# Optimization experiments

Measured on AMD Instinct MI355X. Metric: run time of the kernel, lower is better.

Reference implementation:

```python
import jax, jax.numpy as jnp
import numpy as np

N_EMBD = 1024
N_HEAD = 16


def setup_inputs() -> dict:
    key = jax.random.key(0)
    k1, k2, k3 = jax.random.split(key, 3)
    B, T, C = 4, 2048, N_EMBD
    x = jax.random.normal(k1, (B, T, C), dtype=jnp.float32)
    # params (bias=False)
    w_attn = jax.random.normal(k2, (C, 3 * C), dtype=jnp.float32) * (C ** -0.5)
    w_proj = jax.random.normal(k3, (C, C), dtype=jnp.float32) * (C ** -0.5)
    return {"x": x, "w_attn": w_attn, "w_proj": w_proj}


def reference(x, w_attn, w_proj):
    B, T, C = x.shape
    H = N_HEAD
    hs = C // H
    qkv = x @ w_attn  # [B,T,3C]
    q, k, v = jnp.split(qkv, 3, axis=-1)
    # [B,H,T,hs]
    q = q.reshape(B, T, H, hs).transpose(0, 2, 1, 3)
    k = k.reshape(B, T, H, hs).transpose(0, 2, 1, 3)
    v = v.reshape(B, T, H, hs).transpose(0, 2, 1, 3)
    wei = jnp.einsum('bhqd,bhkd->bhqk', q, k) * (hs ** -0.5)
    causal = jnp.tril(jnp.ones((T, T), dtype=bool))
    wei = jnp.where(causal[None, None], wei, -jnp.inf)
    wei = jax.nn.softmax(wei, axis=-1)
    # dropout p=0.0 -> identity
    y = jnp.einsum('bhqk,bhkd->bhqd', wei, v)
    y = y.transpose(0, 2, 1, 3).reshape(B, T, C)
    return y @ w_proj
```

## Files before the change

kernel.cpp:

```cpp
#include <hip/hip_runtime.h>
#include <math.h>
#include <stdint.h>

#define B_BATCH 4
#define T_SEQ   2048
#define C_EMB   1024
#define NH      16
#define HS      64

typedef _Float16 half_t;
typedef __attribute__((ext_vector_type(8))) _Float16 half8;
typedef __attribute__((ext_vector_type(4))) _Float16 half4;
typedef __attribute__((ext_vector_type(2))) __fp16 pk16x2;
typedef __attribute__((ext_vector_type(4))) float f32x4;

static __device__ __forceinline__ f32x4 mfma_k16(half4 a, half4 b, f32x4 c) {
#if __has_builtin(__builtin_amdgcn_mfma_f32_16x16x16f16)
    return __builtin_amdgcn_mfma_f32_16x16x16f16(a, b, c, 0, 0, 0);
#else
    half8 a8 = {a.x, a.y, a.z, a.w, (_Float16)0, (_Float16)0, (_Float16)0, (_Float16)0};
    half8 b8 = {b.x, b.y, b.z, b.w, (_Float16)0, (_Float16)0, (_Float16)0, (_Float16)0};
    return __builtin_amdgcn_mfma_f32_16x16x32_f16(a8, b8, c, 0, 0, 0);
#endif
}

static __device__ __forceinline__ void stage16(const void* g, void* lds_base) {
#if __has_builtin(__builtin_amdgcn_global_load_lds)
    __builtin_amdgcn_global_load_lds(
        (const __attribute__((address_space(1))) void*)g,
        (__attribute__((address_space(3))) void*)lds_base, 16, 0, 0);
#else
    const int lane = threadIdx.x & 63;
    ((uint4*)lds_base)[lane] = *(const uint4*)g;
#endif
}

__global__ __launch_bounds__(256) void prep_kernel(const float* __restrict__ x,
                                                   half_t* __restrict__ xh,
                                                   const float* __restrict__ wa,
                                                   half_t* __restrict__ waT,
                                                   const float* __restrict__ wp,
                                                   half_t* __restrict__ wpT) {
    const int blk = blockIdx.x;
    const int tid = threadIdx.x;

    if (blk < 4096) {
        const int i = blk * 256 + tid;
        const float4 a = *(const float4*)(x + (size_t)i * 8);
        const float4 b = *(const float4*)(x + (size_t)i * 8 + 4);
        const pk16x2 h0 = __builtin_amdgcn_cvt_pkrtz(a.x, a.y);
        const pk16x2 h1 = __builtin_amdgcn_cvt_pkrtz(a.z, a.w);
        const pk16x2 h2 = __builtin_amdgcn_cvt_pkrtz(b.x, b.y);
        const pk16x2 h3 = __builtin_amdgcn_cvt_pkrtz(b.z, b.w);
        half8 o = {(_Float16)h0.x, (_Float16)h0.y, (_Float16)h1.x, (_Float16)h1.y,
                   (_Float16)h2.x, (_Float16)h2.y, (_Float16)h3.x, (_Float16)h3.y};
        *(half8*)(xh + (size_t)i * 8) = o;
        return;
    }

    const float* W;
    half_t* WT;
    int K, N, bb;
    if (blk < 4096 + 768) {
        bb = blk - 4096; W = wa; WT = waT; K = 1024; N = 3072;
    } else {
        bb = blk - 4864; W = wp; WT = wpT; K = 1024; N = 1024;
    }
    const int ntiles = N / 64;
    const int n0 = (bb % ntiles) * 64;
    const int k0 = (bb / ntiles) * 64;

    __shared__ float t[64][65];
    const int r = tid >> 4, c4 = (tid & 15) * 4;
#pragma unroll
    for (int p = 0; p < 4; ++p) {
        const float4 g = *(const float4*)(W + (size_t)(k0 + p * 16 + r) * N + n0 + c4);
        t[p * 16 + r][c4 + 0] = g.x;
        t[p * 16 + r][c4 + 1] = g.y;
        t[p * 16 + r][c4 + 2] = g.z;
        t[p * 16 + r][c4 + 3] = g.w;
    }
    __syncthreads();
#pragma unroll
    for (int p = 0; p < 4; ++p) {
        const int n = p * 16 + r;
        half4 s = {(_Float16)t[c4 + 0][n], (_Float16)t[c4 + 1][n],
                   (_Float16)t[c4 + 2][n], (_Float16)t[c4 + 3][n]};
        *(half4*)(WT + (size_t)(n0 + n) * K + k0 + c4) = s;
    }
}

#define BK2 64

__global__ __launch_bounds__(512, 2) void gemm256(const half_t* __restrict__ A,
                                                  const half_t* __restrict__ Bt,
                                                  half_t* __restrict__ Cout,
                                                  int M, int N, int K) {
    __shared__ __align__(16) half_t SM[65536];

    const int tid  = threadIdx.x;
    const int lane = tid & 63;
    const int wid  = tid >> 6;
    const int l16  = lane & 15;
    const int quad = lane >> 4;

    const int nwg = gridDim.x;
    const int cpx = nwg >> 3;
    const int bid = (blockIdx.x & 7) * cpx + (blockIdx.x >> 3);
    const int nbx = N >> 8;
    const int bx = bid % nbx;
    const int by = bid / nbx;
    const size_t m0 = (size_t)by << 8;
    const size_t n0 = (size_t)bx << 8;

    const int warpM = (wid >> 2) * 128;
    const int wn    = (wid & 3) * 64;
    const int NTk   = K >> 6;

    const int srow = tid >> 3;
    const int scsw = (tid & 7) ^ (srow & 7);
    const half_t* gAs = A  + (m0 + srow) * (size_t)K + scsw * 8;
    const half_t* gBs = Bt + (n0 + srow) * (size_t)K + scsw * 8;

    f32x4 acc[8][4];
#pragma unroll
    for (int i = 0; i < 8; ++i)
#pragma unroll
        for (int j = 0; j < 4; ++j) acc[i][j] = (f32x4){0.f, 0.f, 0.f, 0.f};

    auto ldA = [&](const half_t* Ab, int mt, int kk) -> half8 {
        const int r = warpM + mt * 16 + l16;
        const int c = (kk * 4 + quad) ^ (l16 & 7);
        return *(const half8*)(Ab + r * 64 + c * 8);
    };
    auto ldB = [&](const half_t* Bb, int nt, int kk) -> half8 {
        const int r = wn + nt * 16 + l16;
        const int c = (kk * 4 + quad) ^ (l16 & 7);
        return *(const half8*)(Bb + r * 64 + c * 8);
    };

#pragma unroll
    for (int s = 0; s < 4; ++s)
        stage16(gAs + (size_t)(s * 64) * K, SM + s * 4096 + wid * 512);
#pragma unroll
    for (int s = 0; s < 4; ++s)
        stage16(gBs + (size_t)(s * 64) * K, SM + 16384 + s * 4096 + wid * 512);
    if (NTk > 1) {
#pragma unroll
        for (int s = 0; s < 4; ++s)
            stage16(gBs + (size_t)(s * 64) * K + BK2, SM + 49152 + s * 4096 + wid * 512);
        asm volatile("s_waitcnt vmcnt(4)" ::: "memory");
    } else {
        asm volatile("s_waitcnt vmcnt(0)" ::: "memory");
    }
    __builtin_amdgcn_s_barrier();
    __builtin_amdgcn_sched_barrier(0);

    auto tile_body = [&](int t, half_t* Ac, half_t* Bc, half_t* An) {
        const int kA = (t + 1) * BK2;
        const int kB = (t + 2) * BK2;
        const bool doA = (t + 1) < NTk;
        const bool doB = (t + 2) < NTk;

        half8 fb[4][2];

        if (doA) {
            stage16(gAs + (size_t)(0 * 64) * K + kA, An + 0 * 4096 + wid * 512);
            stage16(gAs + (size_t)(1 * 64) * K + kA, An + 1 * 4096 + wid * 512);
        }
#pragma unroll
        for (int nt = 0; nt < 4; ++nt) {
            fb[nt][0] = ldB(Bc, nt, 0);
            fb[nt][1] = ldB(Bc, nt, 1);
        }
        {
            half8 a00 = ldA(Ac, 0, 0), a01 = ldA(Ac, 0, 1);
            half8 a10 = ldA(Ac, 1, 0), a11 = ldA(Ac, 1, 1);
            __builtin_amdgcn_s_barrier();
            __builtin_amdgcn_s_setprio(1);
#pragma unroll
            for (int nt = 0; nt < 4; ++nt) {
                acc[0][nt] = __builtin_amdgcn_mfma_f32_16x16x32_f16(a00, fb[nt][0], acc[0][nt], 0, 0, 0);
                acc[0][nt] = __builtin_amdgcn_mfma_f32_16x16x32_f16(a01, fb[nt][1], acc[0][nt], 0, 0, 0);
                acc[1][nt] = __builtin_amdgcn_mfma_f32_16x16x32_f16(a10, fb[nt][0], acc[1][nt], 0, 0, 0);
                acc[1][nt] = __builtin_amdgcn_mfma_f32_16x16x32_f16(a11, fb[nt][1], acc[1][nt], 0, 0, 0);
            }
            __builtin_amdgcn_s_setprio(0);
        }
        if (doA) {
            stage16(gAs + (size_t)(2 * 64) * K + kA, An + 2 * 4096 + wid * 512);
            stage16(gAs + (size_t)(3 * 64) * K + kA, An + 3 * 4096 + wid * 512);
        }
        {
            half8 a00 = ldA(Ac, 2, 0), a01 = ldA(Ac, 2, 1);
            half8 a10 = ldA(Ac, 3, 0), a11 = ldA(Ac, 3, 1);
            __builtin_amdgcn_s_barrier();
            __builtin_amdgcn_s_setprio(1);
#pragma unroll
            for (int nt = 0; nt < 4; ++nt) {
                acc[2][nt] = __builtin_amdgcn_mfma_f32_16x16x32_f16(a00, fb[nt][0], acc[2][nt], 0, 0, 0);
                acc[2][nt] = __builtin_amdgcn_mfma_f32_16x16x32_f16(a01, fb[nt][1], acc[2][nt], 0, 0, 0);
                acc[3][nt] = __builtin_amdgcn_mfma_f32_16x16x32_f16(a10, fb[nt][0], acc[3][nt], 0, 0, 0);
                acc[3][nt] = __builtin_amdgcn_mfma_f32_16x16x32_f16(a11, fb[nt][1], acc[3][nt], 0, 0, 0);
            }
            __builtin_amdgcn_s_setprio(0);
        }
        if (doB) {
            stage16(gBs + (size_t)(0 * 64) * K + kB, Bc + 0 * 4096 + wid * 512);
            stage16(gBs + (size_t)(1 * 64) * K + kB, Bc + 1 * 4096 + wid * 512);
        }
        {
            half8 a00 = ldA(Ac, 4, 0), a01 = ldA(Ac, 4, 1);
            half8 a10 = ldA(Ac, 5, 0), a11 = ldA(Ac, 5, 1);
            __builtin_amdgcn_s_barrier();
            __builtin_amdgcn_s_setprio(1);
#pragma unroll
            for (int nt = 0; nt < 4; ++nt) {
                acc[4][nt] = __builtin_amdgcn_mfma_f32_16x16x32_f16(a00, fb[nt][0], acc[4][nt], 0, 0, 0);
                acc[4][nt] = __builtin_amdgcn_mfma_f32_16x16x32_f16(a01, fb[nt][1], acc[4][nt], 0, 0, 0);
                acc[5][nt] = __builtin_amdgcn_mfma_f32_16x16x32_f16(a10, fb[nt][0], acc[5][nt], 0, 0, 0);
                acc[5][nt] = __builtin_amdgcn_mfma_f32_16x16x32_f16(a11, fb[nt][1], acc[5][nt], 0, 0, 0);
            }
            __builtin_amdgcn_s_setprio(0);
        }
        if (doB) {
            stage16(gBs + (size_t)(2 * 64) * K + kB, Bc + 2 * 4096 + wid * 512);
            stage16(gBs + (size_t)(3 * 64) * K + kB, Bc + 3 * 4096 + wid * 512);
        }
        {
            half8 a00 = ldA(Ac, 6, 0), a01 = ldA(Ac, 6, 1);
            half8 a10 = ldA(Ac, 7, 0), a11 = ldA(Ac, 7, 1);
            __builtin_amdgcn_s_barrier();
            __builtin_amdgcn_s_setprio(1);
#pragma unroll
            for (int nt = 0; nt < 4; ++nt) {
                acc[6][nt] = __builtin_amdgcn_mfma_f32_16x16x32_f16(a00, fb[nt][0], acc[6][nt], 0, 0, 0);
                acc[6][nt] = __builtin_amdgcn_mfma_f32_16x16x32_f16(a01, fb[nt][1], acc[6][nt], 0, 0, 0);
                acc[7][nt] = __builtin_amdgcn_mfma_f32_16x16x32_f16(a10, fb[nt][0], acc[7][nt], 0, 0, 0);
                acc[7][nt] = __builtin_amdgcn_mfma_f32_16x16x32_f16(a11, fb[nt][1], acc[7][nt], 0, 0, 0);
            }
            __builtin_amdgcn_s_setprio(0);
        }
        if (doB) {
            asm volatile("s_waitcnt vmcnt(4)" ::: "memory");
        } else if (doA) {
            asm volatile("s_waitcnt vmcnt(0)" ::: "memory");
        }
        __builtin_amdgcn_s_barrier();
        __builtin_amdgcn_sched_barrier(0);
    };

    for (int tt = 0; tt < NTk; tt += 2) {
        tile_body(tt, SM, SM + 16384, SM + 32768);
        if (tt + 1 < NTk)
            tile_body(tt + 1, SM + 32768, SM + 49152, SM);
    }

    __syncthreads();
    float* cw = (float*)SM + wid * 1024;
    const int rrow = lane >> 2;
    const int cseg = (lane & 3) * 16;
#pragma unroll
    for (int mt = 0; mt < 8; ++mt) {
#pragma unroll
        for (int nt = 0; nt < 4; ++nt)
            *(f32x4*)&cw[(nt * 16 + l16) * 16 + quad * 4] = acc[mt][nt];
        half_t tmp[16];
#pragma unroll
        for (int jj = 0; jj < 16; ++jj)
            tmp[jj] = (half_t)cw[(cseg + jj) * 16 + rrow];
        half_t* dst = Cout + (m0 + warpM + mt * 16 + rrow) * (size_t)N + n0 + wn + cseg;
        *(half8*)(dst)     = *(const half8*)(tmp);
        *(half8*)(dst + 8) = *(const half8*)(tmp + 8);
    }
}

__global__ __launch_bounds__(512, 2) void gemm128f(const half_t* __restrict__ A,
                                                   const half_t* __restrict__ Bt,
                                                   float* __restrict__ Cout,
                                                   int M, int N, int K) {
    __shared__ __align__(16) half_t SM[49152];

    const int tid  = threadIdx.x;
    const int lane = tid & 63;
    const int wid  = tid >> 6;
    const int l16  = lane & 15;
    const int quad = lane >> 4;

    const int nwg = gridDim.x;
    const int cpx = nwg >> 3;
    const int bid = (blockIdx.x & 7) * cpx + (blockIdx.x >> 3);
    const int nbx = N >> 8;
    const int bx = bid % nbx;
    const int by = bid / nbx;
    const size_t m0 = (size_t)by << 7;
    const size_t n0 = (size_t)bx << 8;

    const int warpM = (wid >> 2) * 64;
    const int wn    = (wid & 3) * 64;
    const int NTk   = K >> 6;

    const int srow = tid >> 3;
    const int scsw = (tid & 7) ^ (srow & 7);
    const half_t* gAs = A  + (m0 + srow) * (size_t)K + scsw * 8;
    const half_t* gBs = Bt + (n0 + srow) * (size_t)K + scsw * 8;

    half_t* const A0 = SM;
    half_t* const B0 = SM + 8192;
    half_t* const A1 = SM + 24576;
    half_t* const B1 = SM + 32768;

    f32x4 acc[4][4];
#pragma unroll
    for (int i = 0; i < 4; ++i)
#pragma unroll
        for (int j = 0; j < 4; ++j) acc[i][j] = (f32x4){0.f, 0.f, 0.f, 0.f};

    auto ldA = [&](const half_t* Ab, int mt, int kk) -> half8 {
        const int r = warpM + mt * 16 + l16;
        const int c = (kk * 4 + quad) ^ (l16 & 7);
        return *(const half8*)(Ab + r * 64 + c * 8);
    };
    auto ldB = [&](const half_t* Bb, int nt, int kk) -> half8 {
        const int r = wn + nt * 16 + l16;
        const int c = (kk * 4 + quad) ^ (l16 & 7);
        return *(const half8*)(Bb + r * 64 + c * 8);
    };

#pragma unroll
    for (int s = 0; s < 2; ++s)
        stage16(gAs + (size_t)(s * 64) * K, A0 + s * 4096 + wid * 512);
#pragma unroll
    for (int s = 0; s < 4; ++s)
        stage16(gBs + (size_t)(s * 64) * K, B0 + s * 4096 + wid * 512);
    if (NTk > 1) {
#pragma unroll
        for (int s = 0; s < 4; ++s)
            stage16(gBs + (size_t)(s * 64) * K + BK2, B1 + s * 4096 + wid * 512);
        asm volatile("s_waitcnt vmcnt(4)" ::: "memory");
    } else {
        asm volatile("s_waitcnt vmcnt(0)" ::: "memory");
    }
    __builtin_amdgcn_s_barrier();
    __builtin_amdgcn_sched_barrier(0);

    auto tile_body = [&](int t, half_t* Ac, half_t* Bc, half_t* An) {
        const int kA = (t + 1) * BK2;
        const int kB = (t + 2) * BK2;
        const bool doA = (t + 1) < NTk;
        const bool doB = (t + 2) < NTk;

        half8 fb[4][2];

        if (doA) {
            stage16(gAs + (size_t)(0 * 64) * K + kA, An + 0 * 4096 + wid * 512);
            stage16(gAs + (size_t)(1 * 64) * K + kA, An + 1 * 4096 + wid * 512);
        }
#pragma unroll
        for (int nt = 0; nt < 4; ++nt) {
            fb[nt][0] = ldB(Bc, nt, 0);
            fb[nt][1] = ldB(Bc, nt, 1);
        }
        {
            half8 a00 = ldA(Ac, 0, 0), a01 = ldA(Ac, 0, 1);
            half8 a10 = ldA(Ac, 1, 0), a11 = ldA(Ac, 1, 1);
            __builtin_amdgcn_s_barrier();
            __builtin_amdgcn_s_setprio(1);
#pragma unroll
            for (int nt = 0; nt < 4; ++nt) {
                acc[0][nt] = __builtin_amdgcn_mfma_f32_16x16x32_f16(a00, fb[nt][0], acc[0][nt], 0, 0, 0);
                acc[0][nt] = __builtin_amdgcn_mfma_f32_16x16x32_f16(a01, fb[nt][1], acc[0][nt], 0, 0, 0);
                acc[1][nt] = __builtin_amdgcn_mfma_f32_16x16x32_f16(a10, fb[nt][0], acc[1][nt], 0, 0, 0);
                acc[1][nt] = __builtin_amdgcn_mfma_f32_16x16x32_f16(a11, fb[nt][1], acc[1][nt], 0, 0, 0);
            }
            __builtin_amdgcn_s_setprio(0);
        }
        if (doB) {
#pragma unroll
            for (int s = 0; s < 4; ++s)
                stage16(gBs + (size_t)(s * 64) * K + kB, Bc + s * 4096 + wid * 512);
        }
        {
            half8 a00 = ldA(Ac, 2, 0), a01 = ldA(Ac, 2, 1);
            half8 a10 = ldA(Ac, 3, 0), a11 = ldA(Ac, 3, 1);
            __builtin_amdgcn_s_barrier();
            __builtin_amdgcn_s_setprio(1);
#pragma unroll
            for (int nt = 0; nt < 4; ++nt) {
                acc[2][nt] = __builtin_amdgcn_mfma_f32_16x16x32_f16(a00, fb[nt][0], acc[2][nt], 0, 0, 0);
                acc[2][nt] = __builtin_amdgcn_mfma_f32_16x16x32_f16(a01, fb[nt][1], acc[2][nt], 0, 0, 0);
                acc[3][nt] = __builtin_amdgcn_mfma_f32_16x16x32_f16(a10, fb[nt][0], acc[3][nt], 0, 0, 0);
                acc[3][nt] = __builtin_amdgcn_mfma_f32_16x16x32_f16(a11, fb[nt][1], acc[3][nt], 0, 0, 0);
            }
            __builtin_amdgcn_s_setprio(0);
        }
        if (doB) {
            asm volatile("s_waitcnt vmcnt(4)" ::: "memory");
        } else if (doA) {
            asm volatile("s_waitcnt vmcnt(0)" ::: "memory");
        }
        __builtin_amdgcn_s_barrier();
        __builtin_amdgcn_sched_barrier(0);
    };

    for (int tt = 0; tt < NTk; tt += 2) {
        tile_body(tt, A0, B0, A1);
        if (tt + 1 < NTk)
            tile_body(tt + 1, A1, B1, A0);
    }

#pragma unroll
    for (int mt = 0; mt < 4; ++mt)
#pragma unroll
        for (int nt = 0; nt < 4; ++nt)
#pragma unroll
            for (int r = 0; r < 4; ++r) {
                const size_t row = m0 + warpM + mt * 16 + quad * 4 + r;
                const size_t col = n0 + wn + nt * 16 + l16;
                Cout[row * (size_t)N + col] = acc[mt][nt][r];
            }
}

#define SCALE_EXP2 0.18033688f

__global__ __launch_bounds__(256, 2) void attn_mfma(const half_t* __restrict__ qkv,
                                                    half_t* __restrict__ y) {
    __shared__ __align__(16) half_t Kl[64 * 64];
    __shared__ __align__(16) half_t Vt[64 * 64];
    __shared__ float Lstat[128];

    const int tid  = threadIdx.x;
    const int wid  = tid >> 6;
    const int lane = tid & 63;
    const int l16  = lane & 15;
    const int quad = lane >> 4;

    const int L = blockIdx.x;
    const int g = L & 63;
    const int s = L >> 6;
    const int h = g & 15;
    const int b = g >> 4;

    const size_t rs = 3 * C_EMB;
    const half_t* qb = qkv + (size_t)b * T_SEQ * rs + h * HS;
    const half_t* kb = qb + C_EMB;
    const half_t* vb = qb + 2 * C_EMB;

    const int srow = tid >> 2;
    const int scol = (tid & 3) * 16;
    const int sc2  = (tid & 3) * 2;
    const int rp   = tid & 31;
    const int dblk = tid >> 5;

    const int wq = wid * 32;

    auto kswz = [&](int row, int chunk) -> half_t* {
        return Kl + row * 64 + ((chunk ^ (row & 7)) << 3);
    };
    auto vswz = [&](int row, int chunk) -> half_t* {
        return Vt + row * 64 + ((chunk ^ (row & 7)) << 3);
    };

#pragma unroll 1
    for (int j = 0; j < 2; ++j) {
        const int jj = (j == 0) ? (15 - s) : s;
        const int q0 = jj * 128;
        const int ntk = 2 * jj + 2;

        half8 aQ[2][2];
#pragma unroll
        for (int qs = 0; qs < 2; ++qs)
#pragma unroll
            for (int s2 = 0; s2 < 2; ++s2)
                aQ[qs][s2] = *(const half8*)(qb +
                    (size_t)(q0 + wq + qs * 16 + l16) * rs + s2 * 32 + quad * 8);

        const half_t* kptr = kb + (size_t)srow * rs + scol;
        const half_t* vptr = vb + (size_t)(2 * rp) * rs + dblk * 8;
        half8 kp0, kp1;
        uint4 vpa, vpc;
        kp0 = *(const half8*)(kptr);
        kp1 = *(const half8*)(kptr + 8);
        vpa = *(const uint4*)(vptr);
        vpc = *(const uint4*)(vptr + rs);

        f32x4 O[2][4];
#pragma unroll
        for (int qs = 0; qs < 2; ++qs)
#pragma unroll
            for (int dt = 0; dt < 4; ++dt) O[qs][dt] = (f32x4){0.f, 0.f, 0.f, 0.f};
        float lw[2] = {0.f, 0.f};

        for (int kt = 0; kt < ntk; ++kt) {
            __syncthreads();

            *(half8*)kswz(srow, sc2)     = kp0;
            *(half8*)kswz(srow, sc2 + 1) = kp1;
            {
                const uint32_t a0[4] = {vpa.x, vpa.y, vpa.z, vpa.w};
                const uint32_t c0[4] = {vpc.x, vpc.y, vpc.z, vpc.w};
#pragma unroll
                for (int u = 0; u < 4; ++u) {
                    const int d0 = dblk * 8 + 2 * u;
                    const uint32_t w0 = (a0[u] & 0xffffu) | (c0[u] << 16);
                    const uint32_t w1 = (a0[u] >> 16) | (c0[u] & 0xffff0000u);
                    *(uint32_t*)((unsigned short*)vswz(d0,     rp >> 2) + (rp & 3) * 2) = w0;
                    *(uint32_t*)((unsigned short*)vswz(d0 + 1, rp >> 2) + (rp & 3) * 2) = w1;
                }
            }
            __syncthreads();

            if (kt + 1 < ntk) {
                kptr += 64 * rs;
                vptr += 64 * rs;
                kp0 = *(const half8*)(kptr);
                kp1 = *(const half8*)(kptr + 8);
                vpa = *(const uint4*)(vptr);
                vpc = *(const uint4*)(vptr + rs);
            }

            const bool dmask = (kt >= ntk - 2);

#pragma unroll
            for (int mt = 0; mt < 4; ++mt) {
                const half8 aK0 = *(const half8*)kswz(mt * 16 + l16, quad);
                const half8 aK1 = *(const half8*)kswz(mt * 16 + l16, 4 + quad);
                half4 bV[4];
#pragma unroll
                for (int dt = 0; dt < 4; ++dt)
                    bV[dt] = *(const half4*)(vswz(dt * 16 + l16, 2 * mt + (quad >> 1)) +
                                             (quad & 1) * 4);
                const int kbase = kt * 64 + mt * 16 + quad * 4;
#pragma unroll
                for (int qs = 0; qs < 2; ++qs) {
                    f32x4 sa = (f32x4){0.f, 0.f, 0.f, 0.f};
                    sa = __builtin_amdgcn_mfma_f32_16x16x32_f16(aK0, aQ[qs][0], sa, 0, 0, 0);
                    sa = __builtin_amdgcn_mfma_f32_16x16x32_f16(aK1, aQ[qs][1], sa, 0, 0, 0);

                    float p[4];
#pragma unroll
                    for (int r = 0; r < 4; ++r)
                        p[r] = __builtin_amdgcn_exp2f(sa[r] * SCALE_EXP2);
                    if (dmask) {
                        const int qg = q0 + wq + qs * 16 + l16;
#pragma unroll
                        for (int r = 0; r < 4; ++r)
                            if (kbase + r > qg) p[r] = 0.f;
                    }
                    lw[qs] += (p[0] + p[1]) + (p[2] + p[3]);

                    const half4 pa = {(_Float16)p[0], (_Float16)p[1],
                                      (_Float16)p[2], (_Float16)p[3]};
#pragma unroll
                    for (int dt = 0; dt < 4; ++dt)
                        O[qs][dt] = mfma_k16(pa, bV[dt], O[qs][dt]);
                }
            }
        }

#pragma unroll
        for (int qs = 0; qs < 2; ++qs) {
            lw[qs] += __shfl_xor(lw[qs], 16);
            lw[qs] += __shfl_xor(lw[qs], 32);
            if (quad == 0) Lstat[wq + qs * 16 + l16] = lw[qs];
        }
        __syncthreads();

        if (wid < 2) {
#pragma unroll
            for (int qs = 0; qs < 2; ++qs)
#pragma unroll
                for (int r = 0; r < 4; ++r) {
                    const int rowl = wq + qs * 16 + quad * 4 + r;
                    const float inv = 1.f / Lstat[rowl];
#pragma unroll
                    for (int dt = 0; dt < 4; ++dt)
                        *(vswz(rowl, 2 * dt + (l16 >> 3)) + (l16 & 7)) =
                            (half_t)(O[qs][dt][r] * inv);
                }
        }
        __syncthreads();
        {
            half_t* dst = y + ((size_t)b * T_SEQ + q0 + srow) * C_EMB + h * HS + scol;
            *(half8*)(dst)     = *(const half8*)vswz(srow, sc2);
            *(half8*)(dst + 8) = *(const half8*)vswz(srow, sc2 + 1);
        }
        __syncthreads();

        if (wid >= 2) {
#pragma unroll
            for (int qs = 0; qs < 2; ++qs)
#pragma unroll
                for (int r = 0; r < 4; ++r) {
                    const int rowg = wq + qs * 16 + quad * 4 + r;
                    const float inv = 1.f / Lstat[rowg];
#pragma unroll
                    for (int dt = 0; dt < 4; ++dt)
                        *(vswz(rowg - 64, 2 * dt + (l16 >> 3)) + (l16 & 7)) =
                            (half_t)(O[qs][dt][r] * inv);
                }
        }
        __syncthreads();
        {
            half_t* dst = y + ((size_t)b * T_SEQ + q0 + 64 + srow) * C_EMB + h * HS + scol;
            *(half8*)(dst)     = *(const half8*)vswz(srow, sc2);
            *(half8*)(dst + 8) = *(const half8*)vswz(srow, sc2 + 1);
        }
    }
}

extern "C" void kernel_launch(void* const* d_in, const int* in_sizes, int n_in,
                              void* d_out, int out_size, void* d_ws, size_t ws_size,
                              hipStream_t stream) {
    const float* x      = (const float*)d_in[0];
    const float* w_attn = (const float*)d_in[1];
    const float* w_proj = (const float*)d_in[2];
    float* out = (float*)d_out;

    half_t* xh   = (half_t*)d_ws;
    half_t* waT  = xh   + (size_t)8192 * 1024;
    half_t* wpT  = waT  + (size_t)3072 * 1024;
    half_t* qkvh = wpT  + (size_t)1024 * 1024;
    half_t* yh   = qkvh + (size_t)8192 * 3072;

    prep_kernel<<<5120, 256, 0, stream>>>(x, xh, w_attn, waT, w_proj, wpT);

    gemm256<<<dim3(384), 512, 0, stream>>>(xh, waT, qkvh, 8192, 3072, 1024);

    attn_mfma<<<dim3(512), 256, 0, stream>>>(qkvh, yh);

    gemm128f<<<dim3(256), 512, 0, stream>>>(yh, wpT, out, 8192, 1024, 1024);
}
```

Baseline: 249.1 us.

## Shrink QKV GEMM K-tile to 32 with smaller LDS and simpler schedule

Rewrites the QKV projection GEMM to use a K-step of 32 instead of 64. This halves shared memory to 64KB, raises launch bounds to 4 blocks per CU, changes the LDS swizzle for 32-wide rows, and replaces the four interleaved sub-phases (staggered loads plus barriers) with one load-all-then-MFMA phase per tile. The aim is higher occupancy and fewer barriers. In exchange it doubles the number of K iterations and sync points and loses the fine-grained overlap of global loads with MFMAs. Only 384 blocks are launched, so the extra occupancy may not be usable.

```diff
diff --git a/kernel.cpp b/kernel.cpp
--- a/kernel.cpp
+++ b/kernel.cpp
@@ -90,13 +90,11 @@
     }
 }
 
-#define BK2 64
-
-__global__ __launch_bounds__(512, 2) void gemm256(const half_t* __restrict__ A,
-                                                  const half_t* __restrict__ Bt,
-                                                  half_t* __restrict__ Cout,
-                                                  int M, int N, int K) {
-    __shared__ __align__(16) half_t SM[65536];
+__global__ __launch_bounds__(512, 4) void gemm256k(const half_t* __restrict__ A,
+                                                   const half_t* __restrict__ Bt,
+                                                   half_t* __restrict__ Cout,
+                                                   int M, int N, int K) {
+    __shared__ __align__(16) half_t SM[32768];
 
     const int tid  = threadIdx.x;
     const int lane = tid & 63;
@@ -115,41 +113,43 @@
 
     const int warpM = (wid >> 2) * 128;
     const int wn    = (wid & 3) * 64;
-    const int NTk   = K >> 6;
-
-    const int srow = tid >> 3;
-    const int scsw = (tid & 7) ^ (srow & 7);
+    const int NTk   = K >> 5;
+
+    const int srow = tid >> 2;
+    const int scsw = (tid & 3) ^ ((tid >> 3) & 3);
     const half_t* gAs = A  + (m0 + srow) * (size_t)K + scsw * 8;
     const half_t* gBs = Bt + (n0 + srow) * (size_t)K + scsw * 8;
 
+    half_t* const A0 = SM;
+    half_t* const B0 = SM + 8192;
+    half_t* const A1 = SM + 16384;
+    half_t* const B1 = SM + 24576;
+
     f32x4 acc[8][4];
 #pragma unroll
     for (int i = 0; i < 8; ++i)
 #pragma unroll
         for (int j = 0; j < 4; ++j) acc[i][j] = (f32x4){0.f, 0.f, 0.f, 0.f};
 
-    auto ldA = [&](const half_t* Ab, int mt, int kk) -> half8 {
+    auto ldA = [&](const half_t* Ab, int mt) -> half8 {
         const int r = warpM + mt * 16 + l16;
-        const int c = (kk * 4 + quad) ^ (l16 & 7);
-        return *(const half8*)(Ab + r * 64 + c * 8);
-    };
-    auto ldB = [&](const half_t* Bb, int nt, int kk) -> half8 {
+        const int c = quad ^ ((l16 >> 1) & 3);
+        return *(const half8*)(Ab + r * 32 + c * 8);
+    };
+    auto ldB = [&](const half_t* Bb, int nt) -> half8 {
         const int r = wn + nt * 16 + l16;
-        const int c = (kk * 4 + quad) ^ (l16 & 7);
-        return *(const half8*)(Bb + r * 64 + c * 8);
-    };
-
-#pragma unroll
-    for (int s = 0; s < 4; ++s)
-        stage16(gAs + (size_t)(s * 64) * K, SM + s * 4096 + wid * 512);
-#pragma unroll
-    for (int s = 0; s < 4; ++s)
-        stage16(gBs + (size_t)(s * 64) * K, SM + 16384 + s * 4096 + wid * 512);
+        const int c = quad ^ ((l16 >> 1) & 3);
+        return *(const half8*)(Bb + r * 32 + c * 8);
+    };
+
+    stage16(gAs,                        A0 + wid * 512);
+    stage16(gAs + (size_t)128 * K,      A0 + 4096 + wid * 512);
+    stage16(gBs,                        B0 + wid * 512);
+    stage16(gBs + (size_t)128 * K,      B0 + 4096 + wid * 512);
     if (NTk > 1) {
-#pragma unroll
-        for (int s = 0; s < 4; ++s)
-            stage16(gBs + (size_t)(s * 64) * K + BK2, SM + 49152 + s * 4096 + wid * 512);
-        asm volatile("s_waitcnt vmcnt(4)" ::: "memory");
+        stage16(gBs + 32,                    B1 + wid * 512);
+        stage16(gBs + (size_t)128 * K + 32,  B1 + 4096 + wid * 512);
+        asm volatile("s_waitcnt vmcnt(2)" ::: "memory");
     } else {
         asm volatile("s_waitcnt vmcnt(0)" ::: "memory");
     }
@@ -157,92 +157,36 @@
     __builtin_amdgcn_sched_barrier(0);
 
     auto tile_body = [&](int t, half_t* Ac, half_t* Bc, half_t* An) {
-        const int kA = (t + 1) * BK2;
-        const int kB = (t + 2) * BK2;
+        const int kA = (t + 1) * 32;
+        const int kB = (t + 2) * 32;
         const bool doA = (t + 1) < NTk;
         const bool doB = (t + 2) < NTk;
 
-        half8 fb[4][2];
-
         if (doA) {
-            stage16(gAs + (size_t)(0 * 64) * K + kA, An + 0 * 4096 + wid * 512);
-            stage16(gAs + (size_t)(1 * 64) * K + kA, An + 1 * 4096 + wid * 512);
-        }
-#pragma unroll
-        for (int nt = 0; nt < 4; ++nt) {
-            fb[nt][0] = ldB(Bc, nt, 0);
-            fb[nt][1] = ldB(Bc, nt, 1);
-        }
-        {
-            half8 a00 = ldA(Ac, 0, 0), a01 = ldA(Ac, 0, 1);
-            half8 a10 = ldA(Ac, 1, 0), a11 = ldA(Ac, 1, 1);
-            __builtin_amdgcn_s_barrier();
-            __builtin_amdgcn_s_setprio(1);
-#pragma unroll
-            for (int nt = 0; nt < 4; ++nt) {
-                acc[0][nt] = __builtin_amdgcn_mfma_f32_16x16x32_f16(a00, fb[nt][0], acc[0][nt], 0, 0, 0);
-                acc[0][nt] = __builtin_amdgcn_mfma_f32_16x16x32_f16(a01, fb[nt][1], acc[0][nt], 0, 0, 0);
-                acc[1][nt] = __builtin_amdgcn_mfma_f32_16x16x32_f16(a10, fb[nt][0], acc[1][nt], 0, 0, 0);
-                acc[1][nt] = __builtin_amdgcn_mfma_f32_16x16x32_f16(a11, fb[nt][1], acc[1][nt], 0, 0, 0);
-            }
-            __builtin_amdgcn_s_setprio(0);
-        }
-        if (doA) {
-            stage16(gAs + (size_t)(2 * 64) * K + kA, An + 2 * 4096 + wid * 512);
-            stage16(gAs + (size_t)(3 * 64) * K + kA, An + 3 * 4096 + wid * 512);
-        }
-        {
-            half8 a00 = ldA(Ac, 2, 0), a01 = ldA(Ac, 2, 1);
-            half8 a10 = ldA(Ac, 3, 0), a11 = ldA(Ac, 3, 1);
-            __builtin_amdgcn_s_barrier();
-            __builtin_amdgcn_s_setprio(1);
-#pragma unroll
-            for (int nt = 0; nt < 4; ++nt) {
-                acc[2][nt] = __builtin_amdgcn_mfma_f32_16x16x32_f16(a00, fb[nt][0], acc[2][nt], 0, 0, 0);
-                acc[2][nt] = __builtin_amdgcn_mfma_f32_16x16x32_f16(a01, fb[nt][1], acc[2][nt], 0, 0, 0);
-                acc[3][nt] = __builtin_amdgcn_mfma_f32_16x16x32_f16(a10, fb[nt][0], acc[3][nt], 0, 0, 0);
-                acc[3][nt] = __builtin_amdgcn_mfma_f32_16x16x32_f16(a11, fb[nt][1], acc[3][nt], 0, 0, 0);
-            }
-            __builtin_amdgcn_s_setprio(0);
-        }
+            stage16(gAs + kA,                   An + wid * 512);
+            stage16(gAs + (size_t)128 * K + kA, An + 4096 + wid * 512);
+        }
+        half8 fb[4], fa[8];
+#pragma unroll
+        for (int nt = 0; nt < 4; ++nt) fb[nt] = ldB(Bc, nt);
+#pragma unroll
+        for (int mt = 0; mt < 8; ++mt) fa[mt] = ldA(Ac, mt);
+
+        __builtin_amdgcn_s_setprio(1);
+#pragma unroll
+        for (int mt = 0; mt < 8; ++mt)
+#pragma unroll
+            for (int nt = 0; nt < 4; ++nt)
+                acc[mt][nt] = __builtin_amdgcn_mfma_f32_16x16x32_f16(
+                    fa[mt], fb[nt], acc[mt][nt], 0, 0, 0);
+        __builtin_amdgcn_s_setprio(0);
+
+        __builtin_amdgcn_s_barrier();
+
         if (doB) {
-            stage16(gBs + (size_t)(0 * 64) * K + kB, Bc + 0 * 4096 + wid * 512);
-            stage16(gBs + (size_t)(1 * 64) * K + kB, Bc + 1 * 4096 + wid * 512);
-        }
-        {
-            half8 a00 = ldA(Ac, 4, 0), a01 = ldA(Ac, 4, 1);
-            half8 a10 = ldA(Ac, 5, 0), a11 = ldA(Ac, 5, 1);
-            __builtin_amdgcn_s_barrier();
-            __builtin_amdgcn_s_setprio(1);
-#pragma unroll
-            for (int nt = 0; nt < 4; ++nt) {
-                acc[4][nt] = __builtin_amdgcn_mfma_f32_16x16x32_f16(a00, fb[nt][0], acc[4][nt], 0, 0, 0);
-                acc[4][nt] = __builtin_amdgcn_mfma_f32_16x16x32_f16(a01, fb[nt][1], acc[4][nt], 0, 0, 0);
-                acc[5][nt] = __builtin_amdgcn_mfma_f32_16x16x32_f16(a10, fb[nt][0], acc[5][nt], 0, 0, 0);
-                acc[5][nt] = __builtin_amdgcn_mfma_f32_16x16x32_f16(a11, fb[nt][1], acc[5][nt], 0, 0, 0);
-            }
-            __builtin_amdgcn_s_setprio(0);
-        }
-        if (doB) {
-            stage16(gBs + (size_t)(2 * 64) * K + kB, Bc + 2 * 4096 + wid * 512);
-            stage16(gBs + (size_t)(3 * 64) * K + kB, Bc + 3 * 4096 + wid * 512);
-        }
-        {
-            half8 a00 = ldA(Ac, 6, 0), a01 = ldA(Ac, 6, 1);
-            half8 a10 = ldA(Ac, 7, 0), a11 = ldA(Ac, 7, 1);
-            __builtin_amdgcn_s_barrier();
-            __builtin_amdgcn_s_setprio(1);
-#pragma unroll
-            for (int nt = 0; nt < 4; ++nt) {
-                acc[6][nt] = __builtin_amdgcn_mfma_f32_16x16x32_f16(a00, fb[nt][0], acc[6][nt], 0, 0, 0);
-                acc[6][nt] = __builtin_amdgcn_mfma_f32_16x16x32_f16(a01, fb[nt][1], acc[6][nt], 0, 0, 0);
-                acc[7][nt] = __builtin_amdgcn_mfma_f32_16x16x32_f16(a10, fb[nt][0], acc[7][nt], 0, 0, 0);
-                acc[7][nt] = __builtin_amdgcn_mfma_f32_16x16x32_f16(a11, fb[nt][1], acc[7][nt], 0, 0, 0);
-            }
-            __builtin_amdgcn_s_setprio(0);
-        }
-        if (doB) {
-            asm volatile("s_waitcnt vmcnt(4)" ::: "memory");
+            stage16(gBs + kB,                   Bc + wid * 512);
+            stage16(gBs + (size_t)128 * K + kB, Bc + 4096 + wid * 512);
+            asm volatile("s_waitcnt vmcnt(2)" ::: "memory");
         } else if (doA) {
             asm volatile("s_waitcnt vmcnt(0)" ::: "memory");
         }
@@ -251,9 +195,9 @@
     };
 
     for (int tt = 0; tt < NTk; tt += 2) {
-        tile_body(tt, SM, SM + 16384, SM + 32768);
+        tile_body(tt, A0, B0, A1);
         if (tt + 1 < NTk)
-            tile_body(tt + 1, SM + 32768, SM + 49152, SM);
+            tile_body(tt + 1, A1, B1, A0);
     }
 
     __syncthreads();
@@ -274,6 +218,8 @@
         *(half8*)(dst + 8) = *(const half8*)(tmp + 8);
     }
 }
+
+#define BK2 64
 
 __global__ __launch_bounds__(512, 2) void gemm128f(const half_t* __restrict__ A,
                                                    const half_t* __restrict__ Bt,
@@ -625,7 +571,7 @@
 
     prep_kernel<<<5120, 256, 0, stream>>>(x, xh, w_attn, waT, w_proj, wpT);
 
-    gemm256<<<dim3(384), 512, 0, stream>>>(xh, waT, qkvh, 8192, 3072, 1024);
+    gemm256k<<<dim3(384), 512, 0, stream>>>(xh, waT, qkvh, 8192, 3072, 1024);
 
     attn_mfma<<<dim3(512), 256, 0, stream>>>(qkvh, yh);
 
```

Measured after the change: 721.3 us. +189.6%, slower.

## Double-buffer K/V tiles in LDS for attention kernel, one barrier per step

Applied to the files above, without the earlier changes.

Splits the K and V shared-memory tiles into two buffers so the next tile is written to LDS while the current one is consumed by MFMAs. This cuts the per-iteration barriers from two to one and overlaps LDS stores with compute. In exchange it doubles the K/V LDS footprint, to about 32KB per block, which could reduce occupancy. The register prefetch now runs two tiles ahead.

```diff
diff --git a/kernel.cpp b/kernel.cpp
--- a/kernel.cpp
+++ b/kernel.cpp
@@ -425,8 +425,8 @@
 
 __global__ __launch_bounds__(256, 2) void attn_mfma(const half_t* __restrict__ qkv,
                                                     half_t* __restrict__ y) {
-    __shared__ __align__(16) half_t Kl[64 * 64];
-    __shared__ __align__(16) half_t Vt[64 * 64];
+    __shared__ __align__(16) half_t Kl[2][64 * 64];
+    __shared__ __align__(16) half_t Vt[2][64 * 64];
     __shared__ float Lstat[128];
 
     const int tid  = threadIdx.x;
@@ -454,11 +454,11 @@
 
     const int wq = wid * 32;
 
-    auto kswz = [&](int row, int chunk) -> half_t* {
-        return Kl + row * 64 + ((chunk ^ (row & 7)) << 3);
-    };
-    auto vswz = [&](int row, int chunk) -> half_t* {
-        return Vt + row * 64 + ((chunk ^ (row & 7)) << 3);
+    auto kswz = [&](int bf, int row, int chunk) -> half_t* {
+        return Kl[bf] + row * 64 + ((chunk ^ (row & 7)) << 3);
+    };
+    auto vswz = [&](int bf, int row, int chunk) -> half_t* {
+        return Vt[bf] + row * 64 + ((chunk ^ (row & 7)) << 3);
     };
 
 #pragma unroll 1
@@ -484,6 +484,36 @@
         vpa = *(const uint4*)(vptr);
         vpc = *(const uint4*)(vptr + rs);
 
+        auto writeK = [&](int bf) {
+            *(half8*)kswz(bf, srow, sc2)     = kp0;
+            *(half8*)kswz(bf, srow, sc2 + 1) = kp1;
+        };
+        auto writeV = [&](int bf) {
+            const uint32_t a0[4] = {vpa.x, vpa.y, vpa.z, vpa.w};
+            const uint32_t c0[4] = {vpc.x, vpc.y, vpc.z, vpc.w};
+#pragma unroll
+            for (int u = 0; u < 4; ++u) {
+                const int d0 = dblk * 8 + 2 * u;
+                const uint32_t w0 = (a0[u] & 0xffffu) | (c0[u] << 16);
+                const uint32_t w1 = (a0[u] >> 16) | (c0[u] & 0xffff0000u);
+                *(uint32_t*)((unsigned short*)vswz(bf, d0,     rp >> 2) + (rp & 3) * 2) = w0;
+                *(uint32_t*)((unsigned short*)vswz(bf, d0 + 1, rp >> 2) + (rp & 3) * 2) = w1;
+            }
+        };
+
+        __syncthreads();
+        writeK(0);
+        writeV(0);
+        if (ntk > 1) {
+            kptr += 64 * rs;
+            vptr += 64 * rs;
+            kp0 = *(const half8*)(kptr);
+            kp1 = *(const half8*)(kptr + 8);
+            vpa = *(const uint4*)(vptr);
+            vpc = *(const uint4*)(vptr + rs);
+        }
+        __syncthreads();
+
         f32x4 O[2][4];
 #pragma unroll
         for (int qs = 0; qs < 2; ++qs)
@@ -491,44 +521,31 @@
             for (int dt = 0; dt < 4; ++dt) O[qs][dt] = (f32x4){0.f, 0.f, 0.f, 0.f};
         float lw[2] = {0.f, 0.f};
 
+        int cur = 0;
         for (int kt = 0; kt < ntk; ++kt) {
-            __syncthreads();
-
-            *(half8*)kswz(srow, sc2)     = kp0;
-            *(half8*)kswz(srow, sc2 + 1) = kp1;
-            {
-                const uint32_t a0[4] = {vpa.x, vpa.y, vpa.z, vpa.w};
-                const uint32_t c0[4] = {vpc.x, vpc.y, vpc.z, vpc.w};
-#pragma unroll
-                for (int u = 0; u < 4; ++u) {
-                    const int d0 = dblk * 8 + 2 * u;
-                    const uint32_t w0 = (a0[u] & 0xffffu) | (c0[u] << 16);
-                    const uint32_t w1 = (a0[u] >> 16) | (c0[u] & 0xffff0000u);
-                    *(uint32_t*)((unsigned short*)vswz(d0,     rp >> 2) + (rp & 3) * 2) = w0;
-                    *(uint32_t*)((unsigned short*)vswz(d0 + 1, rp >> 2) + (rp & 3) * 2) = w1;
+            if (kt + 1 < ntk) {
+                writeK(cur ^ 1);
+                writeV(cur ^ 1);
+                if (kt + 2 < ntk) {
+                    kptr += 64 * rs;
+                    vptr += 64 * rs;
+                    kp0 = *(const half8*)(kptr);
+                    kp1 = *(const half8*)(kptr + 8);
+                    vpa = *(const uint4*)(vptr);
+                    vpc = *(const uint4*)(vptr + rs);
                 }
             }
-            __syncthreads();
-
-            if (kt + 1 < ntk) {
-                kptr += 64 * rs;
-                vptr += 64 * rs;
-                kp0 = *(const half8*)(kptr);
-                kp1 = *(const half8*)(kptr + 8);
-                vpa = *(const uint4*)(vptr);
-                vpc = *(const uint4*)(vptr + rs);
-            }
 
             const bool dmask = (kt >= ntk - 2);
 
 #pragma unroll
             for (int mt = 0; mt < 4; ++mt) {
-                const half8 aK0 = *(const half8*)kswz(mt * 16 + l16, quad);
-                const half8 aK1 = *(const half8*)kswz(mt * 16 + l16, 4 + quad);
+                const half8 aK0 = *(const half8*)kswz(cur, mt * 16 + l16, quad);
+                const half8 aK1 = *(const half8*)kswz(cur, mt * 16 + l16, 4 + quad);
                 half4 bV[4];
 #pragma unroll
                 for (int dt = 0; dt < 4; ++dt)
-                    bV[dt] = *(const half4*)(vswz(dt * 16 + l16, 2 * mt + (quad >> 1)) +
+                    bV[dt] = *(const half4*)(vswz(cur, dt * 16 + l16, 2 * mt + (quad >> 1)) +
                                              (quad & 1) * 4);
                 const int kbase = kt * 64 + mt * 16 + quad * 4;
 #pragma unroll
@@ -556,6 +573,9 @@
                         O[qs][dt] = mfma_k16(pa, bV[dt], O[qs][dt]);
                 }
             }
+
+            __syncthreads();
+            cur ^= 1;
         }
 
 #pragma unroll
@@ -575,15 +595,15 @@
                     const float inv = 1.f / Lstat[rowl];
 #pragma unroll
                     for (int dt = 0; dt < 4; ++dt)
-                        *(vswz(rowl, 2 * dt + (l16 >> 3)) + (l16 & 7)) =
+                        *(vswz(0, rowl, 2 * dt + (l16 >> 3)) + (l16 & 7)) =
                             (half_t)(O[qs][dt][r] * inv);
                 }
         }
         __syncthreads();
         {
             half_t* dst = y + ((size_t)b * T_SEQ + q0 + srow) * C_EMB + h * HS + scol;
-            *(half8*)(dst)     = *(const half8*)vswz(srow, sc2);
-            *(half8*)(dst + 8) = *(const half8*)vswz(srow, sc2 + 1);
+            *(half8*)(dst)     = *(const half8*)vswz(0, srow, sc2);
+            *(half8*)(dst + 8) = *(const half8*)vswz(0, srow, sc2 + 1);
         }
         __syncthreads();
 
@@ -596,15 +616,15 @@
                     const float inv = 1.f / Lstat[rowg];
 #pragma unroll
                     for (int dt = 0; dt < 4; ++dt)
-                        *(vswz(rowg - 64, 2 * dt + (l16 >> 3)) + (l16 & 7)) =
+                        *(vswz(0, rowg - 64, 2 * dt + (l16 >> 3)) + (l16 & 7)) =
                             (half_t)(O[qs][dt][r] * inv);
                 }
         }
         __syncthreads();
         {
             half_t* dst = y + ((size_t)b * T_SEQ + q0 + 64 + srow) * C_EMB + h * HS + scol;
-            *(half8*)(dst)     = *(const half8*)vswz(srow, sc2);
-            *(half8*)(dst + 8) = *(const half8*)vswz(srow, sc2 + 1);
+            *(half8*)(dst)     = *(const half8*)vswz(0, srow, sc2);
+            *(half8*)(dst + 8) = *(const half8*)vswz(0, srow, sc2 + 1);
         }
     }
 }
```

Result: slower. 255.2 us (+2.5%).
